# Performance work log

Measured on AMD Instinct MI355X. Metric: run time of the kernel, lower is better.

## Reference

```python
import jax, jax.numpy as jnp
import numpy as np

B, S, D = 2, 2048, 2048
H = 16
HD = D // H

def setup_inputs() -> dict:
    key = jax.random.key(0)
    ks = jax.random.split(key, 6)
    s = 1.0 / np.sqrt(D)
    return {
        "inputs": jax.random.normal(ks[0], (B, S, D), dtype=jnp.float32),
        "w_q": jax.random.normal(ks[1], (D, D), dtype=jnp.float32) * s,
        "w_k": jax.random.normal(ks[2], (D, D), dtype=jnp.float32) * s,
        "w_v": jax.random.normal(ks[3], (D, D), dtype=jnp.float32) * s,
        "w_o": jax.random.normal(ks[4], (D, D), dtype=jnp.float32) * s,
        "b_o": jax.random.normal(ks[5], (D,), dtype=jnp.float32) * 0.02,
    }

def reference(inputs, w_q, w_k, w_v, w_o, b_o):
    b, t, _ = inputs.shape
    # Linear layers: y = x @ W^T (weights stored torch-style [out, in])
    q = (inputs @ w_q.T).reshape(b, t, H, HD)
    k = (inputs @ w_k.T).reshape(b, t, H, HD)
    v = (inputs @ w_v.T).reshape(b, t, H, HD)
    # scores: [b, h, t, t]
    scores = jnp.einsum('bqhd,bkhd->bhqk', q, k)
    causal = jnp.triu(jnp.ones((t, t), dtype=bool), k=1)
    scores = jnp.where(causal, -jnp.inf, scores)
    # NOTE: source scales by sqrt(token_num) (keys.shape[2] after transpose), not sqrt(head_dim)
    scale = jnp.float32(t) ** 0.5
    attn = jax.nn.softmax(scores / scale, axis=-1)
    ctx = jnp.einsum('bhqk,bkhd->bqhd', attn, v).reshape(b, t, D)
    return ctx @ w_o.T + b_o
```

## Files before the change

kernel.cpp:

```cpp
#include <hip/hip_runtime.h>


typedef __attribute__((ext_vector_type(8))) short short8;
typedef __attribute__((ext_vector_type(4))) float f32x4;

#define SEQ 2048
#define DM  2048
#define NHD 128
#define NT  32
#define QSCALE (0.022097086912079608f * 1.4426950408889634f)

#define EXP2F(x) __builtin_amdgcn_exp2f(x)
#define WAITV(N) asm volatile("s_waitcnt vmcnt(" #N ")" ::: "memory")

__device__ __forceinline__ unsigned short f2bf(float f) {
  unsigned u = __builtin_bit_cast(unsigned, f);
  u += 0x7FFFu + ((u >> 16) & 1u);
  return (unsigned short)(u >> 16);
}
__device__ __forceinline__ unsigned short f2bf_fast(float f) {
  unsigned u = __builtin_bit_cast(unsigned, f);
  return (unsigned short)((u + 0x8000u) >> 16);
}

__device__ __forceinline__ void gll16(const void* g, void* l) {
  __builtin_amdgcn_global_load_lds((const __attribute__((address_space(1))) void*)g,
                                   (__attribute__((address_space(3))) void*)l, 16, 0, 0);
}

template <int CTRL>
__device__ __forceinline__ float dpp_mv(float x) {
  int xi = __builtin_bit_cast(int, x);
  return __builtin_bit_cast(float,
      __builtin_amdgcn_update_dpp(xi, xi, CTRL, 0xF, 0xF, false));
}
__device__ __forceinline__ float red16_max(float x) {
  x = fmaxf(x, dpp_mv<0xB1>(x));
  x = fmaxf(x, dpp_mv<0x4E>(x));
  x = fmaxf(x, dpp_mv<0x124>(x));
  x = fmaxf(x, dpp_mv<0x128>(x));
  return x;
}
__device__ __forceinline__ float red16_sum(float x) {
  x += dpp_mv<0xB1>(x);
  x += dpp_mv<0x4E>(x);
  x += dpp_mv<0x124>(x);
  x += dpp_mv<0x128>(x);
  return x;
}

__global__ __launch_bounds__(256) void cast_bf16_k(const float* __restrict__ in,
                                                   unsigned short* __restrict__ out,
                                                   int n8) {
  int i = blockIdx.x * 256 + threadIdx.x;
  if (i >= n8) return;
  const f32x4* p = (const f32x4*)in + (size_t)i * 2;
  f32x4 a = p[0], b = p[1];
  short8 o;
  o[0] = (short)f2bf(a[0]); o[1] = (short)f2bf(a[1]);
  o[2] = (short)f2bf(a[2]); o[3] = (short)f2bf(a[3]);
  o[4] = (short)f2bf(b[0]); o[5] = (short)f2bf(b[1]);
  o[6] = (short)f2bf(b[2]); o[7] = (short)f2bf(b[3]);
  *(short8*)(out + (size_t)i * 8) = o;
}

__global__ __launch_bounds__(256) void cast_w4_k(const float* __restrict__ Wq,
                                                 const float* __restrict__ Wk,
                                                 const float* __restrict__ Wv,
                                                 const float* __restrict__ Wo,
                                                 unsigned short* __restrict__ Wqb,
                                                 unsigned short* __restrict__ Wkb,
                                                 unsigned short* __restrict__ Wvb,
                                                 unsigned short* __restrict__ Wob) {
  int i = blockIdx.x * 256 + threadIdx.x;
  int r = i >> 19, j = i & 524287;
  const float* src = (r == 0) ? Wq : (r == 1) ? Wk : (r == 2) ? Wv : Wo;
  unsigned short* dst = (r == 0) ? Wqb : (r == 1) ? Wkb : (r == 2) ? Wvb : Wob;
  float sc = (r == 0) ? QSCALE : 1.0f;
  const f32x4* p = (const f32x4*)src + (size_t)j * 2;
  f32x4 a = p[0], b = p[1];
  short8 o;
  o[0] = (short)f2bf(a[0] * sc); o[1] = (short)f2bf(a[1] * sc);
  o[2] = (short)f2bf(a[2] * sc); o[3] = (short)f2bf(a[3] * sc);
  o[4] = (short)f2bf(b[0] * sc); o[5] = (short)f2bf(b[1] * sc);
  o[6] = (short)f2bf(b[2] * sc); o[7] = (short)f2bf(b[3] * sc);
  *(short8*)(dst + (size_t)j * 8) = o;
}

__device__ __forceinline__ void stage_half(const unsigned short* __restrict__ gbase,
                                           unsigned short* lhalf, int tid) {
#pragma unroll
  for (int c = 0; c < 2; ++c) {
    int G = c * 512 + tid;
    int row = G >> 3, g = G & 7;
    int gs = g ^ (row & 7);
    gll16(gbase + (size_t)row * DM + gs * 8, lhalf + (size_t)G * 8);
  }
}

#define LOADAF(MH)                                                              \
  _Pragma("unroll") for (int mi = 0; mi < 4; ++mi)                              \
    _Pragma("unroll") for (int ks = 0; ks < 2; ++ks) {                          \
      int row = wm * 64 + mi * 16 + lr;                                         \
      af[mi][ks] = *(const short8*)&lA[(MH) * 8192 + row * 64 +                 \
                                       (((ks * 4 + kb) ^ (row & 7)) * 8)];      \
    }

#define PHASE(MH, NH, STG, WV)                                                  \
  {                                                                             \
    const unsigned short* lBh = lB + (NH) * 8192;                               \
    short8 bfr[2][2];                                                           \
    _Pragma("unroll") for (int ni = 0; ni < 2; ++ni)                            \
      _Pragma("unroll") for (int ks = 0; ks < 2; ++ks) {                        \
        int row = wn * 32 + ni * 16 + lr;                                       \
        bfr[ni][ks] = *(const short8*)&lBh[row * 64 + (((ks * 4 + kb) ^ (row & 7)) * 8)]; \
      }                                                                         \
    STG;                                                                        \
    __builtin_amdgcn_s_barrier();                                               \
    __builtin_amdgcn_s_setprio(1);                                              \
    _Pragma("unroll") for (int mi = 0; mi < 4; ++mi)                            \
      _Pragma("unroll") for (int ni = 0; ni < 2; ++ni) {                        \
        acc[MH][NH][mi][ni] = __builtin_amdgcn_mfma_f32_16x16x32_bf16(          \
            af[mi][0], bfr[ni][0], acc[MH][NH][mi][ni], 0, 0, 0);               \
        acc[MH][NH][mi][ni] = __builtin_amdgcn_mfma_f32_16x16x32_bf16(          \
            af[mi][1], bfr[ni][1], acc[MH][NH][mi][ni], 0, 0, 0);               \
      }                                                                         \
    __builtin_amdgcn_s_setprio(0);                                              \
    WV;                                                                         \
    __builtin_amdgcn_s_barrier();                                               \
  }

__device__ __forceinline__ void gemm256_core(const unsigned short* __restrict__ A,
                                             const unsigned short* __restrict__ B,
                                             unsigned short* LA, unsigned short* LB,
                                             f32x4 acc[2][2][4][2], int m0, int n0) {
  const int tid = threadIdx.x;
  const int w = tid >> 6, l = tid & 63;
  const int lr = l & 15, kb = l >> 4;
  const int wm = w >> 2, wn = w & 3;

  stage_half(A + (size_t)m0 * DM, LA, tid);
  stage_half(B + (size_t)n0 * DM, LB, tid);
  stage_half(B + (size_t)n0 * DM + (size_t)128 * DM, LB + 8192, tid);
  stage_half(A + (size_t)m0 * DM + (size_t)128 * DM, LA + 8192, tid);
  WAITV(4);
  __builtin_amdgcn_s_barrier();

#pragma unroll 1
  for (int t = 0; t < NT; ++t) {
    const unsigned short* lA = LA + (t & 1) * 16384;
    const unsigned short* lB = LB + (t & 1) * 16384;
    unsigned short* sA = LA + ((t + 1) & 1) * 16384;
    unsigned short* sB = LB + ((t + 1) & 1) * 16384;
    const unsigned short* gA = A + (size_t)m0 * DM + (t + 1) * 64;
    const unsigned short* gB = B + (size_t)n0 * DM + (t + 1) * 64;
    const bool st = (t + 1 < NT);
    short8 af[4][2];
    LOADAF(0);
    PHASE(0, 0, if (st) stage_half(gA, sA, tid),
                if (st) { WAITV(4); } else { WAITV(2); });
    PHASE(0, 1, if (st) stage_half(gB, sB, tid),
                if (st) { WAITV(4); } else { WAITV(0); });
    LOADAF(1);
    PHASE(1, 0, if (st) stage_half(gB + (size_t)128 * DM, sB + 8192, tid), );
    PHASE(1, 1, if (st) stage_half(gA + (size_t)128 * DM, sA + 8192, tid),
                if (st) { WAITV(4); });
  }
}

__global__ __launch_bounds__(512, 2) void gemm_qk_k(const unsigned short* __restrict__ X,
                                                    const unsigned short* __restrict__ Wq,
                                                    const unsigned short* __restrict__ Wk,
                                                    unsigned short* __restrict__ Qo,
                                                    unsigned short* __restrict__ Ko) {
  __shared__ unsigned short LA[32768];
  __shared__ unsigned short LB[32768];
  const int lin = blockIdx.x + 8 * (blockIdx.y + 16 * blockIdx.z);
  const int c = lin & 7, idx = lin >> 3;
  const int xb = (c & 1) * 4 + ((idx >> 2) & 3);
  const int yb = (c >> 1) * 4 + (idx & 3);
  const int zb = idx >> 4;
  const unsigned short* W = zb ? Wk : Wq;
  unsigned short* Y = zb ? Ko : Qo;
  const int m0 = yb * 256, n0 = xb * 256;
  const int tid = threadIdx.x, w = tid >> 6, l = tid & 63;
  const int lr = l & 15, kb = l >> 4;
  const int wm = w >> 2, wn = w & 3;
  f32x4 acc[2][2][4][2] = {};
  gemm256_core(X, W, LA, LB, acc, m0, n0);
#pragma unroll
  for (int mh = 0; mh < 2; ++mh)
#pragma unroll
    for (int nh = 0; nh < 2; ++nh)
#pragma unroll
      for (int mi = 0; mi < 4; ++mi)
#pragma unroll
        for (int ni = 0; ni < 2; ++ni)
#pragma unroll
          for (int rr = 0; rr < 4; ++rr) {
            int row = m0 + mh * 128 + wm * 64 + mi * 16 + kb * 4 + rr;
            int col = n0 + nh * 128 + wn * 32 + ni * 16 + lr;
            Y[(size_t)row * DM + col] = f2bf(acc[mh][nh][mi][ni][rr]);
          }
}

#define PH2(NH, STG, WV)                                                        \
  {                                                                             \
    const unsigned short* lBh = lB + (NH) * 8192;                               \
    short8 bfr[2][2];                                                           \
    _Pragma("unroll") for (int ni = 0; ni < 2; ++ni)                            \
      _Pragma("unroll") for (int ks = 0; ks < 2; ++ks) {                        \
        int row = wn * 32 + ni * 16 + lr;                                       \
        bfr[ni][ks] = *(const short8*)&lBh[row * 64 + (((ks * 4 + kb) ^ (row & 7)) * 8)]; \
      }                                                                         \
    STG;                                                                        \
    __builtin_amdgcn_s_barrier();                                               \
    __builtin_amdgcn_s_setprio(1);                                              \
    _Pragma("unroll") for (int mi = 0; mi < 4; ++mi)                            \
      _Pragma("unroll") for (int ni = 0; ni < 2; ++ni) {                        \
        acc[NH][mi][ni] = __builtin_amdgcn_mfma_f32_16x16x32_bf16(              \
            af[mi][0], bfr[ni][0], acc[NH][mi][ni], 0, 0, 0);                   \
        acc[NH][mi][ni] = __builtin_amdgcn_mfma_f32_16x16x32_bf16(              \
            af[mi][1], bfr[ni][1], acc[NH][mi][ni], 0, 0, 0);                   \
      }                                                                         \
    __builtin_amdgcn_s_setprio(0);                                              \
    WV;                                                                         \
    __builtin_amdgcn_s_barrier();                                               \
  }

__device__ __forceinline__ void gemm128x256_core(const unsigned short* __restrict__ A,
                                                 const unsigned short* __restrict__ B,
                                                 unsigned short* LA, unsigned short* LB,
                                                 f32x4 acc[2][4][2], int m0, int n0) {
  const int tid = threadIdx.x;
  const int w = tid >> 6, l = tid & 63;
  const int lr = l & 15, kb = l >> 4;
  const int wm = w >> 2, wn = w & 3;

  stage_half(A + (size_t)m0 * DM, LA, tid);
  stage_half(B + (size_t)n0 * DM, LB, tid);
  stage_half(B + (size_t)n0 * DM + (size_t)128 * DM, LB + 8192, tid);
  WAITV(2);
  __builtin_amdgcn_s_barrier();

#pragma unroll 1
  for (int t = 0; t < NT; ++t) {
    const unsigned short* lA = LA + (t & 1) * 8192;
    const unsigned short* lB = LB + (t & 1) * 16384;
    unsigned short* sA = LA + ((t + 1) & 1) * 8192;
    unsigned short* sB = LB + ((t + 1) & 1) * 16384;
    const unsigned short* gA = A + (size_t)m0 * DM + (t + 1) * 64;
    const unsigned short* gB = B + (size_t)n0 * DM + (t + 1) * 64;
    const bool st = (t + 1 < NT);
    short8 af[4][2];
#pragma unroll
    for (int mi = 0; mi < 4; ++mi)
#pragma unroll
      for (int ks = 0; ks < 2; ++ks) {
        int row = wm * 64 + mi * 16 + lr;
        af[mi][ks] = *(const short8*)&lA[row * 64 + (((ks * 4 + kb) ^ (row & 7)) * 8)];
      }
    PH2(0, if (st) stage_half(gA, sA, tid),
           if (st) { WAITV(2); } else { WAITV(0); });
    PH2(1, if (st) { stage_half(gB, sB, tid); stage_half(gB + (size_t)128 * DM, sB + 8192, tid); },
           if (st) { WAITV(2); });
  }
}

__global__ __launch_bounds__(512, 2) void gemm_vt_k(const unsigned short* __restrict__ Wv,
                                                    const unsigned short* __restrict__ X,
                                                    unsigned short* __restrict__ Vt) {
  __shared__ unsigned short LA[16384];
  __shared__ unsigned short LB[32768];
  const int lin = blockIdx.x + 16 * blockIdx.y;
  const int c = lin & 7, idx = lin >> 3;
  const int yb = (c >> 2) * 8 + (idx & 7);
  const int xb = (c & 3) * 4 + (idx >> 3);
  const int m0 = yb * 128, n0 = xb * 256;
  const int tid = threadIdx.x, w = tid >> 6, l = tid & 63;
  const int lr = l & 15, kb = l >> 4;
  const int wm = w >> 2, wn = w & 3;
  f32x4 acc[2][4][2] = {};
  gemm128x256_core(Wv, X, LA, LB, acc, m0, n0);
#pragma unroll
  for (int nh = 0; nh < 2; ++nh)
#pragma unroll
    for (int mi = 0; mi < 4; ++mi)
#pragma unroll
      for (int ni = 0; ni < 2; ++ni)
#pragma unroll
        for (int rr = 0; rr < 4; ++rr) {
          int i = m0 + wm * 64 + mi * 16 + kb * 4 + rr;
          int j = n0 + nh * 128 + wn * 32 + ni * 16 + lr;
          Vt[((size_t)(j >> 11) * 2048 + i) * 2048 + (j & 2047)] = f2bf(acc[nh][mi][ni][rr]);
        }
}

__global__ __launch_bounds__(512, 2) void gemm_o_k(const unsigned short* __restrict__ A,
                                                   const unsigned short* __restrict__ W,
                                                   const float* __restrict__ bias,
                                                   float* __restrict__ Y) {
  __shared__ unsigned short LA[16384];
  __shared__ unsigned short LB[32768];
  const int lin = blockIdx.x + 8 * blockIdx.y;
  const int c = lin & 7, idx = lin >> 3;
  const int yb = (c >> 1) * 8 + (idx & 7);
  const int xb = (c & 1) * 4 + (idx >> 3);
  const int m0 = yb * 128, n0 = xb * 256;
  const int tid = threadIdx.x, w = tid >> 6, l = tid & 63;
  const int lr = l & 15, kb = l >> 4;
  const int wm = w >> 2, wn = w & 3;
  f32x4 acc[2][4][2] = {};
  gemm128x256_core(A, W, LA, LB, acc, m0, n0);
#pragma unroll
  for (int nh = 0; nh < 2; ++nh)
#pragma unroll
    for (int mi = 0; mi < 4; ++mi)
#pragma unroll
      for (int ni = 0; ni < 2; ++ni)
#pragma unroll
        for (int rr = 0; rr < 4; ++rr) {
          int row = m0 + wm * 64 + mi * 16 + kb * 4 + rr;
          int col = n0 + nh * 128 + wn * 32 + ni * 16 + lr;
          Y[(size_t)row * DM + col] = acc[nh][mi][ni][rr] + bias[col];
        }
}

__device__ __forceinline__ void stage_tiles8(const unsigned short* __restrict__ Kh,
                                             const unsigned short* __restrict__ Vh,
                                             unsigned short* KL, unsigned short* VL,
                                             int kv0, int t) {
#pragma unroll
  for (int c = 0; c < 2; ++c) {
    int S = c * 512 + t;
    int row = S >> 4, g = (S & 15) ^ (row & 7);
    gll16(Kh + (size_t)(kv0 + row) * DM + g * 8, KL + (size_t)S * 8);
  }
#pragma unroll
  for (int c = 0; c < 2; ++c) {
    int S = c * 512 + t;
    int d = S >> 3, g = (S & 7) ^ (d & 7);
    gll16(Vh + (size_t)d * SEQ + kv0 + g * 8, VL + (size_t)S * 8);
  }
}

__device__ __forceinline__ void attn_tile(const unsigned short* __restrict__ Kc,
                                          const unsigned short* __restrict__ Vc,
                                          unsigned short* __restrict__ Pw,
                                          const short8 qf[4], f32x4 ctx[8],
                                          float mrow[4], float lrow[4],
                                          int qw, int kv0, int lr, int kb) {
  f32x4 s[4];
#pragma unroll
  for (int ct = 0; ct < 4; ++ct) {
    s[ct] = (f32x4){0.f, 0.f, 0.f, 0.f};
    int krow = ct * 16 + lr;
#pragma unroll
    for (int ks = 0; ks < 4; ++ks) {
      short8 bf = *(const short8*)&Kc[krow * 128 + (((ks * 4 + kb) ^ (krow & 7)) * 8)];
      s[ct] = __builtin_amdgcn_mfma_f32_16x16x32_bf16(qf[ks], bf, s[ct], 0, 0, 0);
    }
  }
  const bool needmask = (kv0 + 63 > qw);
  float pe[4][4];
#pragma unroll
  for (int r = 0; r < 4; ++r) {
    const int qi = qw + kb * 4 + r;
    float mx = -3.0e4f;
#pragma unroll
    for (int ct = 0; ct < 4; ++ct) {
      float v = s[ct][r];
      if (needmask && (kv0 + ct * 16 + lr > qi)) v = -3.0e4f;
      s[ct][r] = v;
      mx = fmaxf(mx, v);
    }
    mx = red16_max(mx);
    if (mx > mrow[r] + 8.f) {
      float alpha = EXP2F(mrow[r] - mx);
      mrow[r] = mx;
      lrow[r] *= alpha;
#pragma unroll
      for (int cc = 0; cc < 8; ++cc) ctx[cc][r] *= alpha;
    }
    float rs = 0.f;
#pragma unroll
    for (int ct = 0; ct < 4; ++ct) {
      float e = EXP2F(s[ct][r] - mrow[r]);
      pe[ct][r] = e;
      rs += e;
    }
    lrow[r] += red16_sum(rs);
  }
#pragma unroll
  for (int ct = 0; ct < 4; ++ct)
#pragma unroll
    for (int r = 0; r < 4; ++r) {
      int prow = kb * 4 + r;
      int g = (ct * 2 + (lr >> 3)) ^ ((prow >> 1) & 7);
      Pw[prow * 64 + g * 8 + (lr & 7)] = f2bf_fast(pe[ct][r]);
    }
  short8 pa[2];
#pragma unroll
  for (int ks = 0; ks < 2; ++ks)
    pa[ks] = *(const short8*)&Pw[lr * 64 + (((ks * 4 + kb) ^ ((lr >> 1) & 7)) * 8)];
#pragma unroll
  for (int cc = 0; cc < 8; ++cc) {
    int vrow = cc * 16 + lr;
#pragma unroll
    for (int ks = 0; ks < 2; ++ks) {
      short8 vb = *(const short8*)&Vc[vrow * 64 + (((ks * 4 + kb) ^ (vrow & 7)) * 8)];
      ctx[cc] = __builtin_amdgcn_mfma_f32_16x16x32_bf16(pa[ks], vb, ctx[cc], 0, 0, 0);
    }
  }
}

__global__ __launch_bounds__(512) void attn_k(const unsigned short* __restrict__ Q,
                                              const unsigned short* __restrict__ K,
                                              const unsigned short* __restrict__ Vt,
                                              unsigned short* __restrict__ O) {
  __shared__ unsigned short KL[2][64 * 128];
  __shared__ unsigned short VL[2][128 * 64];
  __shared__ unsigned short Pb[8][16 * 64];
  const int t = threadIdx.x, w = t >> 6, l = t & 63;
  const int lr = l & 15, kb = l >> 4;
  const int id = blockIdx.x;
  const int xcd = id & 7, s = id >> 3;
  const int bh = xcd * 4 + (s & 3);
  const int yh = s >> 2;
  const int y = (yh < 8) ? yh : (23 - yh);
  const int b = bh >> 4, h = bh & 15;
  const unsigned short* Kh = K + (size_t)b * SEQ * DM + h * NHD;
  const unsigned short* Vh = Vt + (size_t)bh * NHD * SEQ;

  const int qw = y * 128 + w * 16;
  const int nkt = 2 * y + 2;

  short8 qf[4];
  {
    const unsigned short* qp = Q + (size_t)(b * SEQ + qw + lr) * DM + h * NHD + kb * 8;
#pragma unroll
    for (int ks = 0; ks < 4; ++ks) qf[ks] = *(const short8*)(qp + ks * 32);
  }
  f32x4 ctx[8] = {};
  float mrow[4], lrow[4];
#pragma unroll
  for (int r = 0; r < 4; ++r) { mrow[r] = -3.0e4f; lrow[r] = 0.f; }

  stage_tiles8(Kh, Vh, KL[0], VL[0], 0, t);
  __syncthreads();

  int cbuf = 0;
#pragma unroll 1
  for (int kt = 0; kt < nkt; ++kt) {
    const int kv0 = kt * 64;
    if (kt + 1 < nkt) stage_tiles8(Kh, Vh, KL[cbuf ^ 1], VL[cbuf ^ 1], kv0 + 64, t);
    if (kv0 <= qw + 15)
      attn_tile(KL[cbuf], VL[cbuf], Pb[w], qf, ctx, mrow, lrow, qw, kv0, lr, kb);
    __syncthreads();
    cbuf ^= 1;
  }

#pragma unroll
  for (int r = 0; r < 4; ++r) {
    float inv = 1.f / lrow[r];
    size_t rowoff = (size_t)(b * SEQ + qw + kb * 4 + r) * DM + h * NHD;
#pragma unroll
    for (int cc = 0; cc < 8; ++cc)
      O[rowoff + cc * 16 + lr] = f2bf_fast(ctx[cc][r] * inv);
  }
}

extern "C" void kernel_launch(void* const* d_in, const int* in_sizes, int n_in,
                              void* d_out, int out_size, void* d_ws, size_t ws_size,
                              hipStream_t stream) {
  const float* X  = (const float*)d_in[0];
  const float* Wq = (const float*)d_in[1];
  const float* Wk = (const float*)d_in[2];
  const float* Wv = (const float*)d_in[3];
  const float* Wo = (const float*)d_in[4];
  const float* bo = (const float*)d_in[5];
  float* out = (float*)d_out;

  unsigned short* ws = (unsigned short*)d_ws;
  unsigned short* Xb  = ws;
  unsigned short* Wqb = ws + 8388608;
  unsigned short* Wkb = ws + 12582912;
  unsigned short* Wvb = ws + 16777216;
  unsigned short* Wob = ws + 20971520;
  unsigned short* Qb  = ws + 25165824;
  unsigned short* Kb  = ws + 33554432;
  unsigned short* Vtb = ws + 41943040;
  unsigned short* Cb  = ws + 50331648;

  cast_bf16_k<<<4096, 256, 0, stream>>>(X, Xb, 1048576);
  cast_w4_k<<<8192, 256, 0, stream>>>(Wq, Wk, Wv, Wo, Wqb, Wkb, Wvb, Wob);

  gemm_qk_k<<<dim3(8, 16, 2), 512, 0, stream>>>(Xb, Wqb, Wkb, Qb, Kb);
  gemm_vt_k<<<dim3(16, 16), 512, 0, stream>>>(Wvb, Xb, Vtb);
  attn_k<<<512, 512, 0, stream>>>(Qb, Kb, Vtb, Cb);
  gemm_o_k<<<dim3(8, 32), 512, 0, stream>>>(Cb, Wob, bo, out);
}
```

Before: 251.4 us.

## Fuse cast kernels and defer softmax row-sum reduction in attention

```diff
diff --git a/kernel.cpp b/kernel.cpp
--- a/kernel.cpp
+++ b/kernel.cpp
@@ -49,34 +49,30 @@
   return x;
 }
 
-__global__ __launch_bounds__(256) void cast_bf16_k(const float* __restrict__ in,
-                                                   unsigned short* __restrict__ out,
-                                                   int n8) {
+__global__ __launch_bounds__(256) void cast_all_k(const float* __restrict__ X,
+                                                  const float* __restrict__ Wq,
+                                                  const float* __restrict__ Wk,
+                                                  const float* __restrict__ Wv,
+                                                  const float* __restrict__ Wo,
+                                                  unsigned short* __restrict__ Xb,
+                                                  unsigned short* __restrict__ Wqb,
+                                                  unsigned short* __restrict__ Wkb,
+                                                  unsigned short* __restrict__ Wvb,
+                                                  unsigned short* __restrict__ Wob) {
   int i = blockIdx.x * 256 + threadIdx.x;
-  if (i >= n8) return;
-  const f32x4* p = (const f32x4*)in + (size_t)i * 2;
-  f32x4 a = p[0], b = p[1];
-  short8 o;
-  o[0] = (short)f2bf(a[0]); o[1] = (short)f2bf(a[1]);
-  o[2] = (short)f2bf(a[2]); o[3] = (short)f2bf(a[3]);
-  o[4] = (short)f2bf(b[0]); o[5] = (short)f2bf(b[1]);
-  o[6] = (short)f2bf(b[2]); o[7] = (short)f2bf(b[3]);
-  *(short8*)(out + (size_t)i * 8) = o;
-}
-
-__global__ __launch_bounds__(256) void cast_w4_k(const float* __restrict__ Wq,
-                                                 const float* __restrict__ Wk,
-                                                 const float* __restrict__ Wv,
-                                                 const float* __restrict__ Wo,
-                                                 unsigned short* __restrict__ Wqb,
-                                                 unsigned short* __restrict__ Wkb,
-                                                 unsigned short* __restrict__ Wvb,
-                                                 unsigned short* __restrict__ Wob) {
-  int i = blockIdx.x * 256 + threadIdx.x;
-  int r = i >> 19, j = i & 524287;
-  const float* src = (r == 0) ? Wq : (r == 1) ? Wk : (r == 2) ? Wv : Wo;
-  unsigned short* dst = (r == 0) ? Wqb : (r == 1) ? Wkb : (r == 2) ? Wvb : Wob;
-  float sc = (r == 0) ? QSCALE : 1.0f;
+  const float* src;
+  unsigned short* dst;
+  int j;
+  float sc = 1.0f;
+  if (i < 1048576) {
+    src = X; dst = Xb; j = i;
+  } else {
+    int k = i - 1048576;
+    int r = k >> 19; j = k & 524287;
+    src = (r == 0) ? Wq : (r == 1) ? Wk : (r == 2) ? Wv : Wo;
+    dst = (r == 0) ? Wqb : (r == 1) ? Wkb : (r == 2) ? Wvb : Wob;
+    if (r == 0) sc = QSCALE;
+  }
   const f32x4* p = (const f32x4*)src + (size_t)j * 2;
   f32x4 a = p[0], b = p[1];
   short8 o;
@@ -348,7 +344,7 @@
                                           const unsigned short* __restrict__ Vc,
                                           unsigned short* __restrict__ Pw,
                                           const short8 qf[4], f32x4 ctx[8],
-                                          float mrow[4], float lrow[4],
+                                          float mrow[4], float lpart[4],
                                           int qw, int kv0, int lr, int kb) {
   f32x4 s[4];
 #pragma unroll
@@ -361,35 +357,43 @@
       s[ct] = __builtin_amdgcn_mfma_f32_16x16x32_bf16(qf[ks], bf, s[ct], 0, 0, 0);
     }
   }
-  const bool needmask = (kv0 + 63 > qw);
+  if (kv0 + 63 > qw) {
+#pragma unroll
+    for (int r = 0; r < 4; ++r) {
+      const int qi = qw + kb * 4 + r;
+#pragma unroll
+      for (int ct = 0; ct < 4; ++ct)
+        if (kv0 + ct * 16 + lr > qi) s[ct][r] = -3.0e4f;
+    }
+  }
+  float mxl[4];
+#pragma unroll
+  for (int r = 0; r < 4; ++r)
+    mxl[r] = fmaxf(fmaxf(s[0][r], s[1][r]), fmaxf(s[2][r], s[3][r]));
+  bool hit = (mxl[0] > mrow[0] + 8.f) | (mxl[1] > mrow[1] + 8.f) |
+             (mxl[2] > mrow[2] + 8.f) | (mxl[3] > mrow[3] + 8.f);
+  if (__any(hit)) {
+#pragma unroll
+    for (int r = 0; r < 4; ++r) {
+      float mx = red16_max(mxl[r]);
+      if (mx > mrow[r] + 8.f) {
+        float alpha = EXP2F(mrow[r] - mx);
+        mrow[r] = mx;
+        lpart[r] *= alpha;
+#pragma unroll
+        for (int cc = 0; cc < 8; ++cc) ctx[cc][r] *= alpha;
+      }
+    }
+  }
   float pe[4][4];
 #pragma unroll
   for (int r = 0; r < 4; ++r) {
-    const int qi = qw + kb * 4 + r;
-    float mx = -3.0e4f;
-#pragma unroll
-    for (int ct = 0; ct < 4; ++ct) {
-      float v = s[ct][r];
-      if (needmask && (kv0 + ct * 16 + lr > qi)) v = -3.0e4f;
-      s[ct][r] = v;
-      mx = fmaxf(mx, v);
-    }
-    mx = red16_max(mx);
-    if (mx > mrow[r] + 8.f) {
-      float alpha = EXP2F(mrow[r] - mx);
-      mrow[r] = mx;
-      lrow[r] *= alpha;
-#pragma unroll
-      for (int cc = 0; cc < 8; ++cc) ctx[cc][r] *= alpha;
-    }
-    float rs = 0.f;
 #pragma unroll
     for (int ct = 0; ct < 4; ++ct) {
       float e = EXP2F(s[ct][r] - mrow[r]);
       pe[ct][r] = e;
-      rs += e;
-    }
-    lrow[r] += red16_sum(rs);
+      lpart[r] += e;
+    }
   }
 #pragma unroll
   for (int ct = 0; ct < 4; ++ct)
@@ -442,9 +446,9 @@
     for (int ks = 0; ks < 4; ++ks) qf[ks] = *(const short8*)(qp + ks * 32);
   }
   f32x4 ctx[8] = {};
-  float mrow[4], lrow[4];
-#pragma unroll
-  for (int r = 0; r < 4; ++r) { mrow[r] = -3.0e4f; lrow[r] = 0.f; }
+  float mrow[4], lpart[4];
+#pragma unroll
+  for (int r = 0; r < 4; ++r) { mrow[r] = -3.0e4f; lpart[r] = 0.f; }
 
   stage_tiles8(Kh, Vh, KL[0], VL[0], 0, t);
   __syncthreads();
@@ -455,14 +459,14 @@
     const int kv0 = kt * 64;
     if (kt + 1 < nkt) stage_tiles8(Kh, Vh, KL[cbuf ^ 1], VL[cbuf ^ 1], kv0 + 64, t);
     if (kv0 <= qw + 15)
-      attn_tile(KL[cbuf], VL[cbuf], Pb[w], qf, ctx, mrow, lrow, qw, kv0, lr, kb);
+      attn_tile(KL[cbuf], VL[cbuf], Pb[w], qf, ctx, mrow, lpart, qw, kv0, lr, kb);
     __syncthreads();
     cbuf ^= 1;
   }
 
 #pragma unroll
   for (int r = 0; r < 4; ++r) {
-    float inv = 1.f / lrow[r];
+    float inv = 1.f / red16_sum(lpart[r]);
     size_t rowoff = (size_t)(b * SEQ + qw + kb * 4 + r) * DM + h * NHD;
 #pragma unroll
     for (int cc = 0; cc < 8; ++cc)
@@ -492,8 +496,7 @@
   unsigned short* Vtb = ws + 41943040;
   unsigned short* Cb  = ws + 50331648;
 
-  cast_bf16_k<<<4096, 256, 0, stream>>>(X, Xb, 1048576);
-  cast_w4_k<<<8192, 256, 0, stream>>>(Wq, Wk, Wv, Wo, Wqb, Wkb, Wvb, Wob);
+  cast_all_k<<<12288, 256, 0, stream>>>(X, Wq, Wk, Wv, Wo, Xb, Wqb, Wkb, Wvb, Wob);
 
   gemm_qk_k<<<dim3(8, 16, 2), 512, 0, stream>>>(Xb, Wqb, Wkb, Qb, Kb);
   gemm_vt_k<<<dim3(16, 16), 512, 0, stream>>>(Wvb, Xb, Vtb);
```

Measured after the change: 236.5 us. 1.06x faster.
